# Kernel optimization log

Hardware: AMD Instinct MI355X
Metric: run time of the kernel (lower is better)

The kernel has to match this reference:

```python
import jax, jax.numpy as jnp
import numpy as np

N_NODES = 200000
N_EDGES = 3200000
VOCAB = 10000
D = 25
EPS = 1e-5


def setup_inputs() -> dict:
    key = jax.random.key(0)
    ks = jax.random.split(key, 16)
    x = jax.random.randint(ks[0], (N_NODES,), 0, VOCAB)
    edge_index = jax.random.randint(ks[1], (2, N_EDGES), 0, N_NODES)
    s = 1.0 / np.sqrt(D)
    inp = {
        'x': x,
        'edge_index': edge_index,
        'emb': jax.random.normal(ks[2], (VOCAB, D), jnp.float32),
        'W1': jax.random.normal(ks[3], (D, D), jnp.float32) * s,
        'b1': jnp.zeros((D,), jnp.float32),
        'g1': jnp.ones((D,), jnp.float32),
        'be1': jnp.zeros((D,), jnp.float32),
        'W2': jax.random.normal(ks[4], (D, D), jnp.float32) * s,
        'b2': jnp.zeros((D,), jnp.float32),
        'g2': jnp.ones((D,), jnp.float32),
        'be2': jnp.zeros((D,), jnp.float32),
        'Wm1': jax.random.normal(ks[5], (D, 12), jnp.float32) * s,
        'bm1': jnp.zeros((12,), jnp.float32),
        'Wm2': jax.random.normal(ks[6], (12, 1), jnp.float32) * (1.0 / np.sqrt(12)),
        'bm2': jnp.zeros((1,), jnp.float32),
    }
    return inp


def gcn_conv(h, src, dst, W, b):
    # PyG GCNConv: h @ W, symmetric normalization with self-loops, scatter-add, + bias
    n = h.shape[0]
    h = h @ W
    loops = jnp.arange(n)
    s = jnp.concatenate([src, loops])  # sources j
    d = jnp.concatenate([dst, loops])  # targets i
    deg = jax.ops.segment_sum(jnp.ones_like(d, h.dtype), d, num_segments=n)
    dinv = jnp.where(deg > 0, jax.lax.rsqrt(jnp.maximum(deg, 1.0)), 0.0)
    norm = dinv[s] * dinv[d]  # [E+N]
    msg = h[s] * norm[:, None]
    out = jax.ops.segment_sum(msg, d, num_segments=n)
    return out + b


def batch_norm(h, g, b):
    mu = jnp.mean(h, axis=0)
    var = jnp.mean((h - mu) ** 2, axis=0)
    return (h - mu) * jax.lax.rsqrt(var + EPS) * g + b


def reference(x, edge_index, emb, W1, b1, g1, be1, W2, b2, g2, be2, Wm1, bm1, Wm2, bm2):
    src, dst = edge_index[0], edge_index[1]
    h = emb[x]  # [N, 25]
    h = jax.nn.relu(batch_norm(gcn_conv(h, src, dst, W1, b1), g1, be1))
    h = jax.nn.relu(batch_norm(gcn_conv(h, src, dst, W2, b2), g2, be2))
    h = jax.nn.relu(h @ Wm1 + bm1)
    return jax.nn.sigmoid(h @ Wm2 + bm2)  # [N, 1]
```

## Files before the change

kernel.cpp:

```cpp
#include <hip/hip_runtime.h>
#include <hip/hip_fp16.h>
#include <math.h>

#define D 25
#define PH_STRIDE 32
#define STATS_BLOCKS 512
#define NBKT 512
#define BSH 9
#define BMSK 511
#define BIN_EDGES 8192
#define SORT_CAP 10240
#define NSLOT 64
#define EPS 1e-5f

__global__ __launch_bounds__(256) void binA(const int* __restrict__ dst,
                                            int* __restrict__ hist2D,
                                            float* __restrict__ stPart, int E) {
    if (blockIdx.x < 25) stPart[blockIdx.x * 256 + threadIdx.x] = 0.0f;
    __shared__ int h[NBKT];
    h[threadIdx.x] = 0;
    h[threadIdx.x + 256] = 0;
    __syncthreads();
    int base = blockIdx.x * BIN_EDGES;
#pragma unroll
    for (int j = 0; j < 32; ++j) {
        int idx = base + j * 256 + threadIdx.x;
        if (idx < E) atomicAdd(&h[dst[idx] >> BSH], 1);
    }
    __syncthreads();
    hist2D[blockIdx.x * NBKT + threadIdx.x] = h[threadIdx.x];
    hist2D[blockIdx.x * NBKT + threadIdx.x + 256] = h[threadIdx.x + 256];
}

__global__ __launch_bounds__(512) void colscan(int* __restrict__ hist2D,
                                               int* __restrict__ bCount, int nbBin) {
    __shared__ int s[512];
    int b = blockIdx.x;
    int j = threadIdx.x;
    int v = (j < nbBin) ? hist2D[j * NBKT + b] : 0;
    s[j] = v;
    __syncthreads();
    for (int off = 1; off < 512; off <<= 1) {
        int x = (j >= off) ? s[j - off] : 0;
        __syncthreads();
        s[j] += x;
        __syncthreads();
    }
    if (j < nbBin) hist2D[j * NBKT + b] = s[j] - v;
    if (j == 0) bCount[b] = s[511];
}

__global__ __launch_bounds__(512) void binB(const int* __restrict__ src,
                                            const int* __restrict__ dst,
                                            const int* __restrict__ hist2D,
                                            const int* __restrict__ bCount,
                                            int* __restrict__ binned, int E) {
    __shared__ int rank[NBKT], basew[NBKT], sc[NBKT];
    int t = threadIdx.x;
    int cnt = bCount[t];
    sc[t] = cnt;
    rank[t] = 0;
    __syncthreads();
    for (int off = 1; off < NBKT; off <<= 1) {
        int x = (t >= off) ? sc[t - off] : 0;
        __syncthreads();
        sc[t] += x;
        __syncthreads();
    }
    basew[t] = (sc[t] - cnt) + hist2D[blockIdx.x * NBKT + t];
    __syncthreads();
    int base = blockIdx.x * BIN_EDGES;
#pragma unroll
    for (int j = 0; j < 16; ++j) {
        int idx = base + j * 512 + t;
        if (idx < E) {
            int d = dst[idx];
            int b = d >> BSH;
            int r = atomicAdd(&rank[b], 1);
            binned[basew[b] + r] = (src[idx] << BSH) | (d & BMSK);
        }
    }
}

__global__ __launch_bounds__(512) void bucket_fill(
        const int* __restrict__ binned, const int* __restrict__ bCount,
        int* __restrict__ degi, int* __restrict__ cursor, int* __restrict__ csr, int N) {
    int b = blockIdx.x;
    int nodeBase = b << BSH;
    if (nodeBase >= N) return;
    __shared__ int h[NBKT];
    __shared__ int s2[512];
    __shared__ int sorted[SORT_CAP];
    int t = threadIdx.x;
    s2[t] = (t < b) ? bCount[t] : 0;
    __syncthreads();
    for (int off = 256; off > 0; off >>= 1) {
        if (t < off) s2[t] += s2[t + off];
        __syncthreads();
    }
    int s = s2[0];
    __syncthreads();
    h[t] = 0;
    __syncthreads();
    int cnt = bCount[b];
    int e = s + cnt;
    for (int k = s + t; k < e; k += 512)
        atomicAdd(&h[binned[k] & BMSK], 1);
    __syncthreads();
    int dg = h[t];
    int node = nodeBase + t;
    if (node < N) degi[node] = dg;
    s2[t] = dg;
    __syncthreads();
    for (int off = 1; off < 512; off <<= 1) {
        int x = (t >= off) ? s2[t - off] : 0;
        __syncthreads();
        s2[t] += x;
        __syncthreads();
    }
    int start = s2[t] - dg;
    h[t] = start;
    if (node < N) cursor[node] = s + s2[t];
    __syncthreads();
    if (cnt <= SORT_CAP) {
        for (int k = s + t; k < e; k += 512) {
            int key = binned[k];
            int p = atomicAdd(&h[key & BMSK], 1);
            sorted[p] = key >> BSH;
        }
        __syncthreads();
        for (int j = t; j < cnt; j += 512)
            csr[s + j] = sorted[j];
    } else {
        for (int k = s + t; k < e; k += 512) {
            int key = binned[k];
            int p = atomicAdd(&h[key & BMSK], 1);
            csr[s + p] = key >> BSH;
        }
    }
}

__global__ __launch_bounds__(256) void embed_gemm1_h(
        const int* __restrict__ x, const float* __restrict__ emb,
        const float* __restrict__ W1, const int* __restrict__ degi,
        __half* __restrict__ Ph, int N) {
    __shared__ float sW[D * D];
    for (int j = threadIdx.x; j < D * D; j += blockDim.x) sW[j] = W1[j];
    __syncthreads();
    int i = blockIdx.x * blockDim.x + threadIdx.x;
    if (i >= N) return;
    const float* er = emb + (size_t)x[i] * D;
    float t[D];
#pragma unroll
    for (int k = 0; k < D; ++k) t[k] = er[k];
    float dinv = rsqrtf((float)degi[i] + 1.0f);
    __half* row = Ph + (size_t)i * PH_STRIDE;
#pragma unroll
    for (int d = 0; d < D; ++d) {
        float acc = 0.0f;
#pragma unroll
        for (int k = 0; k < D; ++k) acc = fmaf(t[k], sW[k * D + d], acc);
        row[d] = __float2half(dinv * acc);
    }
#pragma unroll
    for (int d = D; d < PH_STRIDE; ++d) row[d] = __float2half(0.0f);
}

__global__ __launch_bounds__(256) void gather_stats_w8(
        const int* __restrict__ csr, const int* __restrict__ cursor,
        const int* __restrict__ degi, const __half* __restrict__ Ph,
        const float* __restrict__ bias, __half* __restrict__ Qh,
        float* __restrict__ stPart, int N) {
    int t = threadIdx.x;
    int node = blockIdx.x * 16 + (t >> 4);
    int f = t & 15;
    const __half2* rowb = (const __half2*)Ph;
    float q0 = 0.0f, q1 = 0.0f;
    if (node < N) {
        int end = cursor[node];
        int dg = degi[node];
        int k = end - dg;
        float2 sv = __half22float2(rowb[((size_t)node << 4) + f]);
        float ax = sv.x, ay = sv.y;
        for (; k + 8 <= end; k += 8) {
            int s0 = csr[k],     s1 = csr[k + 1], s2 = csr[k + 2], s3 = csr[k + 3];
            int s4 = csr[k + 4], s5 = csr[k + 5], s6 = csr[k + 6], s7 = csr[k + 7];
            float2 v0 = __half22float2(rowb[((size_t)s0 << 4) + f]);
            float2 v1 = __half22float2(rowb[((size_t)s1 << 4) + f]);
            float2 v2 = __half22float2(rowb[((size_t)s2 << 4) + f]);
            float2 v3 = __half22float2(rowb[((size_t)s3 << 4) + f]);
            float2 v4 = __half22float2(rowb[((size_t)s4 << 4) + f]);
            float2 v5 = __half22float2(rowb[((size_t)s5 << 4) + f]);
            float2 v6 = __half22float2(rowb[((size_t)s6 << 4) + f]);
            float2 v7 = __half22float2(rowb[((size_t)s7 << 4) + f]);
            ax += ((v0.x + v1.x) + (v2.x + v3.x)) + ((v4.x + v5.x) + (v6.x + v7.x));
            ay += ((v0.y + v1.y) + (v2.y + v3.y)) + ((v4.y + v5.y) + (v6.y + v7.y));
        }
        for (; k + 4 <= end; k += 4) {
            int s0 = csr[k], s1 = csr[k + 1], s2 = csr[k + 2], s3 = csr[k + 3];
            float2 v0 = __half22float2(rowb[((size_t)s0 << 4) + f]);
            float2 v1 = __half22float2(rowb[((size_t)s1 << 4) + f]);
            float2 v2 = __half22float2(rowb[((size_t)s2 << 4) + f]);
            float2 v3 = __half22float2(rowb[((size_t)s3 << 4) + f]);
            ax += (v0.x + v1.x) + (v2.x + v3.x);
            ay += (v0.y + v1.y) + (v2.y + v3.y);
        }
        for (; k < end; ++k) {
            float2 v = __half22float2(rowb[((size_t)csr[k] << 4) + f]);
            ax += v.x; ay += v.y;
        }
        float dinv = rsqrtf((float)dg + 1.0f);
        if (f < 13) {
            int j0 = f << 1;
            q0 = fmaf(dinv, ax, bias[j0]);
            if (f < 12) q1 = fmaf(dinv, ay, bias[j0 + 1]);
            ((__half2*)Qh)[((size_t)node << 4) + f] = __floats2half2_rn(q0, q1);
        }
    }
    float ls0 = q0, lq0 = q0 * q0, ls1 = q1, lq1 = q1 * q1;
    ls0 += __shfl_down(ls0, 32, 64); ls0 += __shfl_down(ls0, 16, 64);
    lq0 += __shfl_down(lq0, 32, 64); lq0 += __shfl_down(lq0, 16, 64);
    ls1 += __shfl_down(ls1, 32, 64); ls1 += __shfl_down(ls1, 16, 64);
    lq1 += __shfl_down(lq1, 32, 64); lq1 += __shfl_down(lq1, 16, 64);
    __shared__ float red[4][16][4];
    if ((t & 63) < 16) {
        int w = t >> 6;
        red[w][f][0] = ls0; red[w][f][1] = lq0;
        red[w][f][2] = ls1; red[w][f][3] = lq1;
    }
    __syncthreads();
    if (t < 64) {
        int ff = t >> 2, slot = t & 3;
        float tot = red[0][ff][slot] + red[1][ff][slot] + red[2][ff][slot] + red[3][ff][slot];
        int a = 2 * ff + (slot >> 1);
        if (a < D) atomicAdd(&stPart[(blockIdx.x & (NSLOT - 1)) * 50 + a + (slot & 1) * D], tot);
    }
}

__global__ __launch_bounds__(256) void bn_gemm_hp(
        const __half* __restrict__ Qh, const float* __restrict__ stPart, float invN,
        const float* __restrict__ g, const float* __restrict__ be,
        const float* __restrict__ W, const int* __restrict__ degi,
        __half* __restrict__ Ph, int N) {
    __shared__ float sW[D * D];
    __shared__ float sScale[D], sShift[D];
    __shared__ float sSum[2 * D];
    for (int j = threadIdx.x; j < D * D; j += blockDim.x) sW[j] = W[j];
    if (threadIdx.x < 2 * D) {
        float a = 0.0f;
        for (int k = 0; k < NSLOT; ++k) a += stPart[k * 50 + threadIdx.x];
        sSum[threadIdx.x] = a;
    }
    __syncthreads();
    if (threadIdx.x < D) {
        float m = sSum[threadIdx.x] * invN;
        float v = fmaxf(sSum[D + threadIdx.x] * invN - m * m, 0.0f);
        float sc = rsqrtf(v + EPS) * g[threadIdx.x];
        sScale[threadIdx.x] = sc;
        sShift[threadIdx.x] = be[threadIdx.x] - m * sc;
    }
    __syncthreads();
    int i = blockIdx.x * blockDim.x + threadIdx.x;
    if (i >= N) return;
    const __half2* qrow = (const __half2*)Qh + ((size_t)i << 4);
    float t[D];
#pragma unroll
    for (int ff = 0; ff < 13; ++ff) {
        float2 v = __half22float2(qrow[ff]);
        int j0 = ff << 1;
        t[j0] = fmaxf(0.0f, fmaf(v.x, sScale[j0], sShift[j0]));
        if (ff < 12) t[j0 + 1] = fmaxf(0.0f, fmaf(v.y, sScale[j0 + 1], sShift[j0 + 1]));
    }
    float dinv = rsqrtf((float)degi[i] + 1.0f);
    __half* row = Ph + (size_t)i * PH_STRIDE;
#pragma unroll
    for (int d = 0; d < D; ++d) {
        float acc = 0.0f;
#pragma unroll
        for (int k = 0; k < D; ++k) acc = fmaf(t[k], sW[k * D + d], acc);
        row[d] = __float2half(dinv * acc);
    }
#pragma unroll
    for (int d = D; d < PH_STRIDE; ++d) row[d] = __float2half(0.0f);
}

__global__ __launch_bounds__(256) void final_kernel_p(
        const __half* __restrict__ Qh, const float* __restrict__ stPart, float invN,
        const float* __restrict__ g, const float* __restrict__ be,
        const float* __restrict__ Wm1, const float* __restrict__ bm1,
        const float* __restrict__ Wm2, const float* __restrict__ bm2,
        float* __restrict__ out, int N) {
    __shared__ float sW1[D * 12];
    __shared__ float sb1[12], sW2[12];
    __shared__ float sScale[D], sShift[D];
    __shared__ float sSum[2 * D];
    __shared__ float sb2;
    for (int j = threadIdx.x; j < D * 12; j += blockDim.x) sW1[j] = Wm1[j];
    if (threadIdx.x < 12) {
        sb1[threadIdx.x] = bm1[threadIdx.x];
        sW2[threadIdx.x] = Wm2[threadIdx.x];
    }
    if (threadIdx.x < 2 * D) {
        float a = 0.0f;
        for (int k = 0; k < NSLOT; ++k) a += stPart[k * 50 + threadIdx.x];
        sSum[threadIdx.x] = a;
    }
    if (threadIdx.x == 0) sb2 = bm2[0];
    __syncthreads();
    if (threadIdx.x < D) {
        float m = sSum[threadIdx.x] * invN;
        float v = fmaxf(sSum[D + threadIdx.x] * invN - m * m, 0.0f);
        float sc = rsqrtf(v + EPS) * g[threadIdx.x];
        sScale[threadIdx.x] = sc;
        sShift[threadIdx.x] = be[threadIdx.x] - m * sc;
    }
    __syncthreads();
    int i = blockIdx.x * blockDim.x + threadIdx.x;
    if (i >= N) return;
    const __half2* qrow = (const __half2*)Qh + ((size_t)i << 4);
    float t[D];
#pragma unroll
    for (int ff = 0; ff < 13; ++ff) {
        float2 v = __half22float2(qrow[ff]);
        int j0 = ff << 1;
        t[j0] = fmaxf(0.0f, fmaf(v.x, sScale[j0], sShift[j0]));
        if (ff < 12) t[j0 + 1] = fmaxf(0.0f, fmaf(v.y, sScale[j0 + 1], sShift[j0 + 1]));
    }
    float z = sb2;
#pragma unroll
    for (int j = 0; j < 12; ++j) {
        float m = sb1[j];
#pragma unroll
        for (int k = 0; k < D; ++k) m = fmaf(t[k], sW1[k * 12 + j], m);
        m = fmaxf(0.0f, m);
        z = fmaf(m, sW2[j], z);
    }
    out[i] = 1.0f / (1.0f + expf(-z));
}

__global__ void hist_kernel(const int* __restrict__ dst, int* __restrict__ degi, int E) {
    int e = blockIdx.x * blockDim.x + threadIdx.x;
    if (e < E) atomicAdd(&degi[dst[e]], 1);
}

__global__ __launch_bounds__(256) void embed_gemm1(
        const int* __restrict__ x, const float* __restrict__ emb,
        const float* __restrict__ W1, const int* __restrict__ degi,
        float* __restrict__ P, float* __restrict__ Qdup, int N) {
    __shared__ float sW[D * D];
    for (int j = threadIdx.x; j < D * D; j += blockDim.x) sW[j] = W1[j];
    __syncthreads();
    int i = blockIdx.x * blockDim.x + threadIdx.x;
    if (i >= N) return;
    const float* er = emb + (size_t)x[i] * D;
    float t[D];
#pragma unroll
    for (int k = 0; k < D; ++k) t[k] = er[k];
    float dinv = rsqrtf((float)degi[i] + 1.0f);
#pragma unroll
    for (int d = 0; d < D; ++d) {
        float acc = 0.0f;
#pragma unroll
        for (int k = 0; k < D; ++k) acc = fmaf(t[k], sW[k * D + d], acc);
        float v = dinv * acc;
        P[i * D + d] = v;
        if (Qdup) Qdup[i * D + d] = v;
    }
}

__global__ void scatter_kernel(const int* __restrict__ src, const int* __restrict__ dst,
                               const float* __restrict__ A, float* __restrict__ B, int E) {
    int idx = blockIdx.x * blockDim.x + threadIdx.x;
    int e = idx >> 5;
    int lane = idx & 31;
    if (e >= E || lane >= D) return;
    atomicAdd(&B[dst[e] * D + lane], A[src[e] * D + lane]);
}

__global__ __launch_bounds__(256) void transform_kernel(
        float* __restrict__ Q, const int* __restrict__ degi,
        const float* __restrict__ bias, int N) {
    int i = blockIdx.x * blockDim.x + threadIdx.x;
    if (i >= N) return;
    float dinv = rsqrtf((float)degi[i] + 1.0f);
#pragma unroll
    for (int d = 0; d < D; ++d)
        Q[i * D + d] = fmaf(dinv, Q[i * D + d], bias[d]);
}

__global__ __launch_bounds__(256) void stats_kernel(
        const float* __restrict__ Q, float* __restrict__ st, int N) {
    float ls[D], lq[D];
#pragma unroll
    for (int d = 0; d < D; ++d) { ls[d] = 0.0f; lq[d] = 0.0f; }
    for (int i = blockIdx.x * blockDim.x + threadIdx.x; i < N;
         i += gridDim.x * blockDim.x) {
#pragma unroll
        for (int d = 0; d < D; ++d) {
            float v = Q[i * D + d];
            ls[d] += v;
            lq[d] += v * v;
        }
    }
#pragma unroll
    for (int d = 0; d < D; ++d) {
        for (int off = 32; off > 0; off >>= 1) {
            ls[d] += __shfl_down(ls[d], off, 64);
            lq[d] += __shfl_down(lq[d], off, 64);
        }
    }
    __shared__ float red[4][2 * D];
    int wave = threadIdx.x >> 6;
    int lane = threadIdx.x & 63;
    if (lane == 0) {
#pragma unroll
        for (int d = 0; d < D; ++d) {
            red[wave][d] = ls[d];
            red[wave][D + d] = lq[d];
        }
    }
    __syncthreads();
    if (threadIdx.x < 2 * D) {
        float t = red[0][threadIdx.x] + red[1][threadIdx.x] +
                  red[2][threadIdx.x] + red[3][threadIdx.x];
        atomicAdd(&st[threadIdx.x], t);
    }
}

__global__ __launch_bounds__(256) void bn_gemm(
        const float* __restrict__ Qin, const float* __restrict__ st, float invN,
        const float* __restrict__ g, const float* __restrict__ be,
        const float* __restrict__ W, const int* __restrict__ degi,
        float* __restrict__ P, float* __restrict__ Qdup, int N) {
    __shared__ float sW[D * D];
    __shared__ float sScale[D], sShift[D];
    for (int j = threadIdx.x; j < D * D; j += blockDim.x) sW[j] = W[j];
    if (threadIdx.x < D) {
        float m = st[threadIdx.x] * invN;
        float v = fmaxf(st[D + threadIdx.x] * invN - m * m, 0.0f);
        float sc = rsqrtf(v + EPS) * g[threadIdx.x];
        sScale[threadIdx.x] = sc;
        sShift[threadIdx.x] = be[threadIdx.x] - m * sc;
    }
    __syncthreads();
    int i = blockIdx.x * blockDim.x + threadIdx.x;
    if (i >= N) return;
    float t[D];
#pragma unroll
    for (int d = 0; d < D; ++d)
        t[d] = fmaxf(0.0f, fmaf(Qin[i * D + d], sScale[d], sShift[d]));
    float dinv = rsqrtf((float)degi[i] + 1.0f);
#pragma unroll
    for (int d = 0; d < D; ++d) {
        float acc = 0.0f;
#pragma unroll
        for (int k = 0; k < D; ++k) acc = fmaf(t[k], sW[k * D + d], acc);
        float v = dinv * acc;
        P[i * D + d] = v;
        if (Qdup) Qdup[i * D + d] = v;
    }
}

__global__ __launch_bounds__(256) void final_kernel(
        const float* __restrict__ Q, const float* __restrict__ st, float invN,
        const float* __restrict__ g, const float* __restrict__ be,
        const float* __restrict__ Wm1, const float* __restrict__ bm1,
        const float* __restrict__ Wm2, const float* __restrict__ bm2,
        float* __restrict__ out, int N) {
    __shared__ float sW1[D * 12];
    __shared__ float sb1[12], sW2[12];
    __shared__ float sScale[D], sShift[D];
    __shared__ float sb2;
    for (int j = threadIdx.x; j < D * 12; j += blockDim.x) sW1[j] = Wm1[j];
    if (threadIdx.x < 12) {
        sb1[threadIdx.x] = bm1[threadIdx.x];
        sW2[threadIdx.x] = Wm2[threadIdx.x];
    }
    if (threadIdx.x < D) {
        float m = st[threadIdx.x] * invN;
        float v = fmaxf(st[D + threadIdx.x] * invN - m * m, 0.0f);
        float sc = rsqrtf(v + EPS) * g[threadIdx.x];
        sScale[threadIdx.x] = sc;
        sShift[threadIdx.x] = be[threadIdx.x] - m * sc;
    }
    if (threadIdx.x == 0) sb2 = bm2[0];
    __syncthreads();
    int i = blockIdx.x * blockDim.x + threadIdx.x;
    if (i >= N) return;
    float t[D];
#pragma unroll
    for (int d = 0; d < D; ++d)
        t[d] = fmaxf(0.0f, fmaf(Q[i * D + d], sScale[d], sShift[d]));
    float z = sb2;
#pragma unroll
    for (int j = 0; j < 12; ++j) {
        float m = sb1[j];
#pragma unroll
        for (int k = 0; k < D; ++k) m = fmaf(t[k], sW1[k * 12 + j], m);
        m = fmaxf(0.0f, m);
        z = fmaf(m, sW2[j], z);
    }
    out[i] = 1.0f / (1.0f + expf(-z));
}

extern "C" void kernel_launch(void* const* d_in, const int* in_sizes, int n_in,
                              void* d_out, int out_size, void* d_ws, size_t ws_size,
                              hipStream_t stream) {
    const int*   x    = (const int*)d_in[0];
    const int*   ei   = (const int*)d_in[1];
    const float* emb  = (const float*)d_in[2];
    const float* W1   = (const float*)d_in[3];
    const float* b1   = (const float*)d_in[4];
    const float* g1   = (const float*)d_in[5];
    const float* be1  = (const float*)d_in[6];
    const float* W2   = (const float*)d_in[7];
    const float* b2   = (const float*)d_in[8];
    const float* g2   = (const float*)d_in[9];
    const float* be2  = (const float*)d_in[10];
    const float* Wm1  = (const float*)d_in[11];
    const float* bm1  = (const float*)d_in[12];
    const float* Wm2  = (const float*)d_in[13];
    const float* bm2  = (const float*)d_in[14];
    float* out = (float*)d_out;

    int N = in_sizes[0];
    int E = in_sizes[1] / 2;
    const int* src = ei;
    const int* dst = ei + E;
    float invN = 1.0f / (float)N;

    int nbBin = (E + BIN_EDGES - 1) / BIN_EDGES;
    size_t csrNeed = ((size_t)34 * N + E + 512 + (size_t)nbBin * NBKT + 2 * NSLOT * 50) * 4;
    bool useCSR = (ws_size >= csrNeed) && (N <= NBKT * 512) && (nbBin <= 512) &&
                  ((size_t)E <= (size_t)16 * N) && (nbBin >= 25);

    int nbN  = (N + 255) / 256;
    int nbE  = (E + 255) / 256;
    int nbG  = (N + 15) / 16;
    int nbS  = (int)(((long)E * 32 + 255) / 256);

    if (useCSR) {
        int*    degi    = (int*)d_ws;
        int*    cursor  = degi + N;
        int*    csr     = cursor + N;
        int*    bCount  = csr + E;
        int*    hist2D  = bCount + NBKT;
        __half* Ph      = (__half*)(hist2D + (size_t)nbBin * NBKT);
        __half* Qh      = Ph + (size_t)N * PH_STRIDE;
        float*  stP1    = (float*)(Qh + (size_t)N * PH_STRIDE);
        float*  stP2    = stP1 + NSLOT * 50;
        int*    binned  = (int*)Qh;

        int nbBkt = (N + 511) / 512;

        binA<<<nbBin, 256, 0, stream>>>(dst, hist2D, stP1, E);
        colscan<<<NBKT, 512, 0, stream>>>(hist2D, bCount, nbBin);
        binB<<<nbBin, 512, 0, stream>>>(src, dst, hist2D, bCount, binned, E);
        bucket_fill<<<nbBkt, 512, 0, stream>>>(binned, bCount, degi, cursor, csr, N);
        embed_gemm1_h<<<nbN, 256, 0, stream>>>(x, emb, W1, degi, Ph, N);
        gather_stats_w8<<<nbG, 256, 0, stream>>>(csr, cursor, degi, Ph, b1, Qh, stP1, N);
        bn_gemm_hp<<<nbN, 256, 0, stream>>>(Qh, stP1, invN, g1, be1, W2, degi, Ph, N);
        gather_stats_w8<<<nbG, 256, 0, stream>>>(csr, cursor, degi, Ph, b2, Qh, stP2, N);
        final_kernel_p<<<nbN, 256, 0, stream>>>(Qh, stP2, invN, g2, be2, Wm1, bm1, Wm2, bm2, out, N);
    } else {
        int*   degi  = (int*)d_ws;
        float* P     = (float*)(degi + N);
        float* Q     = P + (size_t)N * D;
        float* stats = Q + (size_t)N * D;
        float* st1 = stats;
        float* st2 = stats + 50;

        hipMemsetAsync(degi, 0, (size_t)N * sizeof(int), stream);
        hipMemsetAsync(stats, 0, 100 * sizeof(float), stream);

        hist_kernel<<<nbE, 256, 0, stream>>>(dst, degi, E);
        embed_gemm1<<<nbN, 256, 0, stream>>>(x, emb, W1, degi, P, Q, N);
        scatter_kernel<<<nbS, 256, 0, stream>>>(src, dst, P, Q, E);
        transform_kernel<<<nbN, 256, 0, stream>>>(Q, degi, b1, N);
        stats_kernel<<<STATS_BLOCKS, 256, 0, stream>>>(Q, st1, N);
        bn_gemm<<<nbN, 256, 0, stream>>>(Q, st1, invN, g1, be1, W2, degi, P, Q, N);
        scatter_kernel<<<nbS, 256, 0, stream>>>(src, dst, P, Q, E);
        transform_kernel<<<nbN, 256, 0, stream>>>(Q, degi, b2, N);
        stats_kernel<<<STATS_BLOCKS, 256, 0, stream>>>(Q, st2, N);
        final_kernel<<<nbN, 256, 0, stream>>>(Q, st2, invN, g2, be2, Wm1, bm1, Wm2, bm2, out, N);
    }
}
```

Measured before the change: 308.8 us.

## Fuse CSR build stages into one cooperative kernel with grid syncs

```diff
diff --git a/kernel.cpp b/kernel.cpp
--- a/kernel.cpp
+++ b/kernel.cpp
@@ -1,6 +1,9 @@
 #include <hip/hip_runtime.h>
+#include <hip/hip_cooperative_groups.h>
 #include <hip/hip_fp16.h>
 #include <math.h>
+
+namespace cg = cooperative_groups;
 
 #define D 25
 #define PH_STRIDE 32
@@ -12,6 +15,128 @@
 #define SORT_CAP 10240
 #define NSLOT 64
 #define EPS 1e-5f
+
+__global__ __launch_bounds__(512) void build_coop(
+        const int* __restrict__ src, const int* __restrict__ dst,
+        int* __restrict__ hist2D, int* __restrict__ bCount,
+        int* __restrict__ binned, int* __restrict__ degi,
+        int* __restrict__ cursor, int* __restrict__ csr,
+        float* __restrict__ stPart, int E, int N, int nbBin, int nbBkt) {
+    cg::grid_group grid = cg::this_grid();
+    __shared__ int h[NBKT];
+    __shared__ int s2[NBKT];
+    __shared__ int sorted[SORT_CAP];
+    int t = threadIdx.x;
+
+    for (int c = blockIdx.x; c < nbBin; c += gridDim.x) {
+        h[t] = 0;
+        __syncthreads();
+        int base = c * BIN_EDGES;
+#pragma unroll
+        for (int j = 0; j < 16; ++j) {
+            int idx = base + j * 512 + t;
+            if (idx < E) atomicAdd(&h[dst[idx] >> BSH], 1);
+        }
+        __syncthreads();
+        hist2D[c * NBKT + t] = h[t];
+        __syncthreads();
+    }
+    for (int i = blockIdx.x * 512 + t; i < 2 * NSLOT * 50; i += gridDim.x * 512)
+        stPart[i] = 0.0f;
+    grid.sync();
+
+    for (int b = blockIdx.x; b < NBKT; b += gridDim.x) {
+        int v = (t < nbBin) ? hist2D[t * NBKT + b] : 0;
+        s2[t] = v;
+        __syncthreads();
+        for (int off = 1; off < 512; off <<= 1) {
+            int x = (t >= off) ? s2[t - off] : 0;
+            __syncthreads();
+            s2[t] += x;
+            __syncthreads();
+        }
+        if (t < nbBin) hist2D[t * NBKT + b] = s2[t] - v;
+        if (t == 0) bCount[b] = s2[511];
+        __syncthreads();
+    }
+    grid.sync();
+
+    {
+        int cnt = bCount[t];
+        s2[t] = cnt;
+        __syncthreads();
+        for (int off = 1; off < 512; off <<= 1) {
+            int x = (t >= off) ? s2[t - off] : 0;
+            __syncthreads();
+            s2[t] += x;
+            __syncthreads();
+        }
+        h[t] = s2[t] - cnt;
+        __syncthreads();
+    }
+    for (int c = blockIdx.x; c < nbBin; c += gridDim.x) {
+        s2[t] = 0;
+        sorted[t] = h[t] + hist2D[c * NBKT + t];
+        __syncthreads();
+        int base = c * BIN_EDGES;
+#pragma unroll
+        for (int j = 0; j < 16; ++j) {
+            int idx = base + j * 512 + t;
+            if (idx < E) {
+                int d = dst[idx];
+                int b = d >> BSH;
+                int r = atomicAdd(&s2[b], 1);
+                binned[sorted[b] + r] = (src[idx] << BSH) | (d & BMSK);
+            }
+        }
+        __syncthreads();
+    }
+    grid.sync();
+
+    for (int b = blockIdx.x; b < nbBkt; b += gridDim.x) {
+        int s = h[b];
+        int cnt = bCount[b];
+        int e = s + cnt;
+        s2[t] = 0;
+        __syncthreads();
+        for (int k = s + t; k < e; k += 512)
+            atomicAdd(&s2[binned[k] & BMSK], 1);
+        __syncthreads();
+        int dg = s2[t];
+        int node = (b << BSH) + t;
+        if (node < N) degi[node] = dg;
+        sorted[t] = dg;
+        __syncthreads();
+        for (int off = 1; off < 512; off <<= 1) {
+            int x = (t >= off) ? sorted[t - off] : 0;
+            __syncthreads();
+            sorted[t] += x;
+            __syncthreads();
+        }
+        int rowEnd = sorted[t];
+        if (node < N) cursor[node] = s + rowEnd;
+        __syncthreads();
+        s2[t] = rowEnd - dg;
+        __syncthreads();
+        if (cnt <= SORT_CAP) {
+            for (int k = s + t; k < e; k += 512) {
+                int key = binned[k];
+                int p = atomicAdd(&s2[key & BMSK], 1);
+                sorted[p] = key >> BSH;
+            }
+            __syncthreads();
+            for (int j = t; j < cnt; j += 512)
+                csr[s + j] = sorted[j];
+        } else {
+            for (int k = s + t; k < e; k += 512) {
+                int key = binned[k];
+                int p = atomicAdd(&s2[key & BMSK], 1);
+                csr[s + p] = key >> BSH;
+            }
+        }
+        __syncthreads();
+    }
+}
 
 __global__ __launch_bounds__(256) void binA(const int* __restrict__ dst,
                                             int* __restrict__ hist2D,
@@ -553,10 +678,38 @@
 
         int nbBkt = (N + 511) / 512;
 
-        binA<<<nbBin, 256, 0, stream>>>(dst, hist2D, stP1, E);
-        colscan<<<NBKT, 512, 0, stream>>>(hist2D, bCount, nbBin);
-        binB<<<nbBin, 512, 0, stream>>>(src, dst, hist2D, bCount, binned, E);
-        bucket_fill<<<nbBkt, 512, 0, stream>>>(binned, bCount, degi, cursor, csr, N);
+        int coopOK = 0;
+        {
+            hipDeviceProp_t prop;
+            int dev = 0;
+            if (hipGetDevice(&dev) == hipSuccess &&
+                hipGetDeviceProperties(&prop, dev) == hipSuccess &&
+                prop.cooperativeLaunch) {
+                int occ = 0;
+                if (hipOccupancyMaxActiveBlocksPerMultiprocessor(
+                        &occ, (const void*)build_coop, 512, 0) == hipSuccess && occ > 0) {
+                    int cap = occ * prop.multiProcessorCount;
+                    int want = NBKT;
+                    int grid = (want < cap) ? want : cap;
+                    const int* srcp = src; const int* dstp = dst;
+                    int* h2 = hist2D; int* bc = bCount; int* bn = binned;
+                    int* dg = degi; int* cu = cursor; int* cs = csr;
+                    float* sp = stP1;
+                    int Ev = E, Nv = N, nbBv = nbBin, nbKv = nbBkt;
+                    void* args[] = {&srcp, &dstp, &h2, &bc, &bn, &dg, &cu, &cs,
+                                    &sp, &Ev, &Nv, &nbBv, &nbKv};
+                    if (hipLaunchCooperativeKernel((void*)build_coop, dim3(grid),
+                                                   dim3(512), args, 0, stream) == hipSuccess)
+                        coopOK = 1;
+                }
+            }
+        }
+        if (!coopOK) {
+            binA<<<nbBin, 256, 0, stream>>>(dst, hist2D, stP1, E);
+            colscan<<<NBKT, 512, 0, stream>>>(hist2D, bCount, nbBin);
+            binB<<<nbBin, 512, 0, stream>>>(src, dst, hist2D, bCount, binned, E);
+            bucket_fill<<<nbBkt, 512, 0, stream>>>(binned, bCount, degi, cursor, csr, N);
+        }
         embed_gemm1_h<<<nbN, 256, 0, stream>>>(x, emb, W1, degi, Ph, N);
         gather_stats_w8<<<nbG, 256, 0, stream>>>(csr, cursor, degi, Ph, b1, Qh, stP1, N);
         bn_gemm_hp<<<nbN, 256, 0, stream>>>(Qh, stP1, invN, g1, be1, W2, degi, Ph, N);
```

Result: slower. 432.2 us (+40.0%).
